# Kernel tuning notes

Measured on AMD Instinct MI355X. Metric: run time of the kernel, lower is better.

## Reference

```python
import jax, jax.numpy as jnp
import numpy as np

B, N, T, F_IN, H, OUT = 64, 207, 48, 6, 64, 1
RANK = 24  # fixed inner dim of learned adjacency factors


def setup_inputs() -> dict:
    key = jax.random.key(0)
    ks = jax.random.split(key, 10)
    s = lambda k, shp, sc=1.0: jax.random.normal(k, shp, jnp.float32) * sc
    return {
        "x": s(ks[0], (B, N, T, F_IN)),
        "N1": s(ks[1], (N, RANK)),
        "N2": s(ks[2], (RANK, N)),
        "W1": s(ks[3], (F_IN, H), 0.2),
        "b1": jnp.zeros((H,), jnp.float32),
        "W2": s(ks[4], (H, H), 0.1),
        "b2": jnp.zeros((H,), jnp.float32),
        "W_ih": s(ks[5], (4 * H, H), 0.1),
        "W_hh": s(ks[6], (4 * H, H), 0.1),
        "b_ih": jnp.zeros((4 * H,), jnp.float32),
        "b_hh": jnp.zeros((4 * H,), jnp.float32),
        "W_fc": s(ks[7], (H, OUT), 0.1),
        "b_fc": jnp.zeros((OUT,), jnp.float32),
    }


def reference(x, N1, N2, W1, b1, W2, b2, W_ih, W_hh, b_ih, b_hh, W_fc, b_fc):
    Bn, Nn, Tn, Fn = x.shape
    # sigmoid(N1@N2) > 0 everywhere -> dense_to_sparse yields ALL N^2 edges
    # (self-loops included); GCNConv's gcn_norm adds one extra self-loop,
    # edge weights all 1 -> A = ones + I, deg = N+1, symmetric normalization.
    adj = jax.nn.sigmoid(N1 @ N2)
    mask = (adj > 0).astype(x.dtype)  # structurally all-ones
    A = mask + jnp.eye(Nn, dtype=x.dtype)
    dinv = jax.lax.rsqrt(A.sum(axis=1))
    A_hat = dinv[:, None] * A * dinv[None, :]  # [N, N]

    xt = jnp.transpose(x, (0, 2, 1, 3))  # [B, T, N, F]
    # GCNConv: propagate(x @ W) with sym-norm, then bias; relu; dropout=eval no-op
    h = jax.nn.relu(jnp.einsum('mn,btnh->btmh', A_hat, xt @ W1) + b1)
    h = jax.nn.relu(jnp.einsum('mn,btnh->btmh', A_hat, h @ W2) + b2)

    # [B, T, N, H] -> [B*N, T, H] for the LSTM
    seq = jnp.transpose(h, (0, 2, 1, 3)).reshape(Bn * Nn, Tn, -1)
    Hd = W_hh.shape[1]

    def step(carry, x_t):
        h_prev, c_prev = carry
        g = x_t @ W_ih.T + b_ih + h_prev @ W_hh.T + b_hh
        i, f, gg, o = jnp.split(g, 4, axis=-1)  # torch gate order i,f,g,o
        c = jax.nn.sigmoid(f) * c_prev + jax.nn.sigmoid(i) * jnp.tanh(gg)
        h_new = jax.nn.sigmoid(o) * jnp.tanh(c)
        return (h_new, c), None

    h0 = jnp.zeros((Bn * Nn, Hd), x.dtype)
    (hT, _), _ = jax.lax.scan(step, (h0, h0), jnp.transpose(seq, (1, 0, 2)))
    out = hT @ W_fc + b_fc  # [B*N, OUT]
    return out.reshape(Bn, Nn, -1)
```

## Files before the change

kernel.cpp:

```cpp
#include <hip/hip_runtime.h>
#include <math.h>

#define NB 64
#define NN 207
#define NT 48
#define NF 6
#define NH 64
#define NSEQ (NB*NN)
#define NG   (NSEQ/16)
#define TSU  ((size_t)NSEQ*NH)

typedef short bf8_t __attribute__((ext_vector_type(8)));
typedef float f4_t  __attribute__((ext_vector_type(4)));
typedef unsigned short ushort;
typedef unsigned int uint;

__device__ __forceinline__ ushort bf16h(float x){
  uint u = __float_as_uint(x);
  return (ushort)((u + 0x7FFF + ((u>>16)&1)) >> 16);
}
__device__ __forceinline__ float bf16f(ushort h){
  return __uint_as_float((uint)h << 16);
}
__device__ __forceinline__ float fsig(float x){
  return __builtin_amdgcn_rcpf(1.0f + __expf(-x));
}
__device__ __forceinline__ float ftanh(float x){
  x = fminf(15.0f, fmaxf(-15.0f, x));
  float e = __expf(2.0f*x);
  return 1.0f - 2.0f*__builtin_amdgcn_rcpf(e + 1.0f);
}

__device__ __forceinline__ void lds_barrier(){
  __builtin_amdgcn_sched_barrier(0);
  asm volatile("s_waitcnt lgkmcnt(0)" ::: "memory");
  __builtin_amdgcn_s_barrier();
  __builtin_amdgcn_sched_barrier(0);
}


#define HW 72
#define XS6 40
#define GCN7_LDS_BYTES (208*HW*2 + (207*XS6 + NF*64 + 64 + 64 + 6*64 + 6*64 + 48)*4)

__global__ __launch_bounds__(256, 2) void gcn_kernel(
    const float* __restrict__ x, const float* __restrict__ W1, const float* __restrict__ b1,
    const float* __restrict__ W2, const float* __restrict__ b2,
    ushort* __restrict__ sxh, ushort* __restrict__ sxl)
{
  extern __shared__ char smraw[];
  ushort* h1b = (ushort*)smraw;
  float*  xs6 = (float*)(h1b + 208*HW);
  float*  W1s = xs6 + 207*XS6;
  float*  b1s = W1s + NF*64;
  float*  b2s = b1s + 64;
  float*  S2_ = b2s + 64;
  float*  r1_ = S2_ + 6*64;
  float*  xsA = r1_ + 6*64;

  const int tid = threadIdx.x;
  const int tg = blockIdx.x, b = blockIdx.y;
  const float inv = 1.0f/208.0f;
  const int l = tid & 63;
  const int w = __builtin_amdgcn_readfirstlane(tid >> 6);
  const int col = l & 15, q = l >> 4;
  const int cw = w*16 + col;

  for (int i=tid; i<6*64; i+=256){ S2_[i]=0.f; r1_[i]=0.f; }
  if (tid < 48) xsA[tid] = 0.f;
  if (tid < 72) h1b[207*HW + tid] = 0;

  for (int i=tid;i<NF*64;i+=256) W1s[i]=W1[i];
  if (tid<64){ b1s[tid]=b1[tid]; b2s[tid]=b2[tid]; }
  {
    const float* xb = x + (size_t)b*NN*(NT*NF) + (size_t)tg*36;
    for (int i=tid; i<207*9; i+=256){
      int n = i/9, c = (i - n*9)*4;
      *(float4*)&xs6[n*XS6 + c] = *(const float4*)&xb[(size_t)n*(NT*NF) + c];
    }
  }
  __syncthreads();

  if (tid < 144){
    int tt = tid/24, rem = tid - tt*24, f = rem>>2, p = rem&3;
    float ps = 0.f;
    for (int n=p; n<NN; n+=4) ps += xs6[n*XS6 + tt*6 + f];
    atomicAdd(&xsA[tt*8+f], ps);
  }

  float wtmp[16];
  #pragma unroll
  for (int kc=0;kc<2;kc++)
    #pragma unroll
    for (int j=0;j<8;j++)
      wtmp[kc*8+j] = W2[(size_t)(kc*32 + q*8 + j)*64 + cw];
  bf8_t B2[2];
  #pragma unroll
  for (int kc=0;kc<2;kc++){
    bf8_t ph;
    #pragma unroll
    for (int j=0;j<8;j++) ph[j] = (short)bf16h(wtmp[kc*8+j]);
    B2[kc]=ph;
  }
  __syncthreads();

  const int ht4 = (tid & 15) * 4;
  const int nti = tid >> 4;

  #pragma unroll 1
  for (int tt=0; tt<6; tt++){
    const int t = tg*6 + tt;
    {
      float s1v[4];
      #pragma unroll
      for (int j=0;j<4;j++){
        float a = 0.f;
        #pragma unroll
        for (int f=0;f<NF;f++) a += xsA[tt*8+f]*W1s[f*64 + ht4 + j];
        s1v[j] = a;
      }
      float cs0=0.f, cs1=0.f, cs2=0.f, cs3=0.f;
      #pragma unroll 1
      for (int p=0;p<4;p++){
        int nt = p*16 + nti;
        if (nt < 52){
          #pragma unroll
          for (int i=0;i<4;i++){
            int n = 4*nt+i;
            if (n < NN){
              float a0=0.f,a1=0.f,a2=0.f,a3=0.f;
              #pragma unroll
              for (int f=0;f<NF;f++){
                float xv = xs6[n*XS6 + tt*6 + f];
                float4 wv = *(const float4*)&W1s[f*64 + ht4];
                a0+=xv*wv.x; a1+=xv*wv.y; a2+=xv*wv.z; a3+=xv*wv.w;
              }
              float v0=(a0+s1v[0])*inv + b1s[ht4+0]; v0 = v0>0.f?v0:0.f;
              float v1=(a1+s1v[1])*inv + b1s[ht4+1]; v1 = v1>0.f?v1:0.f;
              float v2=(a2+s1v[2])*inv + b1s[ht4+2]; v2 = v2>0.f?v2:0.f;
              float v3=(a3+s1v[3])*inv + b1s[ht4+3]; v3 = v3>0.f?v3:0.f;
              ushort4 hi;
              hi.x=bf16h(v0); hi.y=bf16h(v1); hi.z=bf16h(v2); hi.w=bf16h(v3);
              *(ushort4*)&h1b[n*HW + ht4] = hi;
              cs0+=v0; cs1+=v1; cs2+=v2; cs3+=v3;
            }
          }
        }
      }
      atomicAdd(&r1_[tt*64+ht4+0], cs0);
      atomicAdd(&r1_[tt*64+ht4+1], cs1);
      atomicAdd(&r1_[tt*64+ht4+2], cs2);
      atomicAdd(&r1_[tt*64+ht4+3], cs3);
    }
    __syncthreads();

    {
      int h = tid & 63, pp = tid >> 6;
      float ps = 0.f;
      #pragma unroll
      for (int k=0;k<16;k++) ps += r1_[tt*64+pp*16+k]*W2[(size_t)(pp*16+k)*64 + h];
      atomicAdd(&S2_[tt*64+h], ps);
    }

    f4_t acc[13];
    #pragma unroll
    for (int mt=0;mt<13;mt++){ f4_t z; z[0]=0.f;z[1]=0.f;z[2]=0.f;z[3]=0.f; acc[mt]=z; }
    #pragma unroll 2
    for (int mt=0;mt<13;mt++){
      #pragma unroll
      for (int kc=0;kc<2;kc++){
        bf8_t ah = *(const bf8_t*)(h1b + (mt*16+col)*HW + kc*32 + q*8);
        acc[mt] = __builtin_amdgcn_mfma_f32_16x16x32_bf16(ah, B2[kc], acc[mt], 0,0,0);
      }
    }
    __syncthreads();

    {
      const float s2v = S2_[tt*64+cw], b2v = b2s[cw];
      const size_t obase = (size_t)t*TSU + (size_t)(b*NN)*NH + cw;
      #pragma unroll
      for (int mt=0;mt<13;mt++){
        #pragma unroll
        for (int r=0;r<4;r++){
          int n = mt*16 + q*4 + r;
          if (n < NN){
            float v = (acc[mt][r] + s2v)*inv + b2v;
            v = v>0.f ? v : 0.f;
            ushort hb = bf16h(v);
            sxh[obase + (size_t)n*NH] = hb;
            sxl[obase + (size_t)n*NH] = bf16h(v - bf16f(hb));
          }
        }
      }
    }
  }
}

#define HS2 72

__global__ __launch_bounds__(256, 2) void lstm17_kernel(
    const ushort* __restrict__ sxh, const ushort* __restrict__ sxl,
    const float* __restrict__ Wih, const float* __restrict__ Whh,
    const float* __restrict__ bih, const float* __restrict__ bhh,
    const float* __restrict__ Wfc, const float* __restrict__ bfc, float* __restrict__ out)
{
  __shared__ __align__(16) ushort hhp[2][16*HS2 + 8];
  __shared__ __align__(16) ushort hlp[2][16*HS2 + 8];

  const int tid = threadIdx.x;
  const int l = tid & 63;
  const int w = __builtin_amdgcn_readfirstlane(tid >> 6);
  const int col = l & 15, q = l >> 4;
  const int g = blockIdx.x;

  bf8_t Bh[4][4], Bl[4][4];
  #pragma unroll
  for (int mat=0; mat<2; mat++){
    const float* W = mat ? Whh : Wih;
    #pragma unroll
    for (int ty=0; ty<4; ty++){
      #pragma unroll
      for (int kk=0; kk<2; kk++){
        const float* wp = W + (size_t)(ty*64 + w*16 + col)*64 + kk*32 + q*8;
        bf8_t ph, pl;
        #pragma unroll
        for (int j=0;j<8;j++){
          float wv = wp[j];
          ushort hb = bf16h(wv);
          ph[j] = (short)hb;
          pl[j] = (short)bf16h(wv - bf16f(hb));
        }
        Bh[ty][mat*2+kk] = ph;
        Bl[ty][mat*2+kk] = pl;
      }
    }
  }
  float bias[4];
  #pragma unroll
  for (int ty=0;ty<4;ty++){
    int r = ty*64 + w*16 + col;
    bias[ty] = bih[r] + bhh[r];
  }
  float c[4];
  #pragma unroll
  for (int i=0;i<4;i++) c[i]=0.f;

  for (int i=tid; i<16*HS2; i+=256){ hhp[0][i] = 0; hlp[0][i] = 0; }

  const ushort* xgh = sxh + (size_t)g*1024 + (size_t)(col*64 + q*8);
  const ushort* xgl = sxl + (size_t)g*1024 + (size_t)(col*64 + q*8);

  bf8_t pxh[2][2], pxl[2][2];
  #pragma unroll
  for (int s2=0; s2<2; s2++){
    const size_t off = (size_t)s2*TSU;
    pxh[s2][0] = *(const bf8_t*)(xgh + off);
    pxh[s2][1] = *(const bf8_t*)(xgh + off + 32);
    pxl[s2][0] = *(const bf8_t*)(xgl + off);
    pxl[s2][1] = *(const bf8_t*)(xgl + off + 32);
  }

  const int d = w*16 + col;
  __syncthreads();

  #pragma unroll 2
  for (int t=0; t<NT; t++){
    const int cur = t & 1;
    bf8_t cxh0 = pxh[cur][0], cxh1 = pxh[cur][1];
    bf8_t cxl0 = pxl[cur][0], cxl1 = pxl[cur][1];
    if (t+2 < NT){
      const size_t off = (size_t)(t+2)*TSU;
      pxh[cur][0] = *(const bf8_t*)(xgh + off);
      pxh[cur][1] = *(const bf8_t*)(xgh + off + 32);
      pxl[cur][0] = *(const bf8_t*)(xgl + off);
      pxl[cur][1] = *(const bf8_t*)(xgl + off + 32);
    }

    f4_t acc[4];
    #pragma unroll
    for (int ty=0;ty<4;ty++){ f4_t z; z[0]=bias[ty];z[1]=bias[ty];z[2]=bias[ty];z[3]=bias[ty]; acc[ty]=z; }
    #pragma unroll
    for (int ty=0;ty<4;ty++){
      acc[ty] = __builtin_amdgcn_mfma_f32_16x16x32_bf16(cxh0, Bh[ty][0], acc[ty], 0,0,0);
      acc[ty] = __builtin_amdgcn_mfma_f32_16x16x32_bf16(cxl0, Bh[ty][0], acc[ty], 0,0,0);
      acc[ty] = __builtin_amdgcn_mfma_f32_16x16x32_bf16(cxh0, Bl[ty][0], acc[ty], 0,0,0);
      acc[ty] = __builtin_amdgcn_mfma_f32_16x16x32_bf16(cxh1, Bh[ty][1], acc[ty], 0,0,0);
      acc[ty] = __builtin_amdgcn_mfma_f32_16x16x32_bf16(cxl1, Bh[ty][1], acc[ty], 0,0,0);
      acc[ty] = __builtin_amdgcn_mfma_f32_16x16x32_bf16(cxh1, Bl[ty][1], acc[ty], 0,0,0);
    }

    lds_barrier();

    bf8_t hh0, hh1, hl0, hl1;
    {
      const ushort* ph = &hhp[cur][0] + col*HS2 + q*8;
      const ushort* pl = &hlp[cur][0] + col*HS2 + q*8;
      hh0 = *(const bf8_t*)(ph);
      hh1 = *(const bf8_t*)(ph + 32);
      hl0 = *(const bf8_t*)(pl);
      hl1 = *(const bf8_t*)(pl + 32);
    }
    #pragma unroll
    for (int ty=0;ty<4;ty++){
      acc[ty] = __builtin_amdgcn_mfma_f32_16x16x32_bf16(hh0, Bh[ty][2], acc[ty], 0,0,0);
      acc[ty] = __builtin_amdgcn_mfma_f32_16x16x32_bf16(hl0, Bh[ty][2], acc[ty], 0,0,0);
      acc[ty] = __builtin_amdgcn_mfma_f32_16x16x32_bf16(hh0, Bl[ty][2], acc[ty], 0,0,0);
      acc[ty] = __builtin_amdgcn_mfma_f32_16x16x32_bf16(hh1, Bh[ty][3], acc[ty], 0,0,0);
      acc[ty] = __builtin_amdgcn_mfma_f32_16x16x32_bf16(hl1, Bh[ty][3], acc[ty], 0,0,0);
      acc[ty] = __builtin_amdgcn_mfma_f32_16x16x32_bf16(hh1, Bl[ty][3], acc[ty], 0,0,0);
    }

    {
      ushort* wh = &hhp[cur^1][0];
      ushort* wl = &hlp[cur^1][0];
      float hv[4];
      #pragma unroll
      for (int r=0;r<4;r++){
        float ig = fsig(acc[0][r]);
        float fg = fsig(acc[1][r]);
        float gt = ftanh(acc[2][r]);
        float og = fsig(acc[3][r]);
        float cc = fg*c[r] + ig*gt;
        c[r] = cc;
        hv[r] = og*ftanh(cc);
      }
      const int o0 = (q*4)*HS2 + d;
      if (t != NT-1){
        uint ph01, ph23, pl01, pl23;
        asm("v_cvt_pk_bf16_f32 %0, %1, %2" : "=v"(ph01) : "v"(hv[0]), "v"(hv[1]));
        asm("v_cvt_pk_bf16_f32 %0, %1, %2" : "=v"(ph23) : "v"(hv[2]), "v"(hv[3]));
        float r0 = hv[0] - __uint_as_float(ph01 << 16);
        float r1 = hv[1] - __uint_as_float(ph01 & 0xffff0000u);
        float r2 = hv[2] - __uint_as_float(ph23 << 16);
        float r3 = hv[3] - __uint_as_float(ph23 & 0xffff0000u);
        asm("v_cvt_pk_bf16_f32 %0, %1, %2" : "=v"(pl01) : "v"(r0), "v"(r1));
        asm("v_cvt_pk_bf16_f32 %0, %1, %2" : "=v"(pl23) : "v"(r2), "v"(r3));
        wh[o0]         = (ushort)ph01;
        wh[o0 + HS2]   = (ushort)(ph01 >> 16);
        wh[o0 + 2*HS2] = (ushort)ph23;
        wh[o0 + 3*HS2] = (ushort)(ph23 >> 16);
        wl[o0]         = (ushort)pl01;
        wl[o0 + HS2]   = (ushort)(pl01 >> 16);
        wl[o0 + 2*HS2] = (ushort)pl23;
        wl[o0 + 3*HS2] = (ushort)(pl23 >> 16);
      } else {
        #pragma unroll
        for (int r=0;r<4;r++){
          uint bits = __float_as_uint(hv[r]);
          wh[o0 + r*HS2] = (ushort)(bits >> 16);
          wl[o0 + r*HS2] = (ushort)(bits & 0xffffu);
        }
      }
    }
  }
  __syncthreads();

  if (tid < 16){
    float a = bfc[0];
    const ushort* fh = &hhp[NT&1][0] + tid*HS2;
    const ushort* fl = &hlp[NT&1][0] + tid*HS2;
    #pragma unroll 8
    for (int k=0;k<64;k++){
      float v = __uint_as_float(((uint)fh[k] << 16) | (uint)fl[k]);
      a += v * Wfc[k];
    }
    out[g*16 + tid] = a;
  }
}

extern "C" void kernel_launch(void* const* d_in, const int* in_sizes, int n_in,
                              void* d_out, int out_size, void* d_ws, size_t ws_size,
                              hipStream_t stream) {
  const float* x   = (const float*)d_in[0];
  const float* W1  = (const float*)d_in[3];
  const float* b1  = (const float*)d_in[4];
  const float* W2  = (const float*)d_in[5];
  const float* b2  = (const float*)d_in[6];
  const float* Wih = (const float*)d_in[7];
  const float* Whh = (const float*)d_in[8];
  const float* bih = (const float*)d_in[9];
  const float* bhh = (const float*)d_in[10];
  const float* Wfc = (const float*)d_in[11];
  const float* bfc = (const float*)d_in[12];

  ushort* sxh = (ushort*)d_ws;
  ushort* sxl = sxh + (size_t)NT*TSU;
  float*  out = (float*)d_out;

  hipFuncSetAttribute((const void*)gcn_kernel, hipFuncAttributeMaxDynamicSharedMemorySize, GCN7_LDS_BYTES);

  gcn_kernel<<<dim3(NT/6, NB), 256, GCN7_LDS_BYTES, stream>>>(x, W1, b1, W2, b2, sxh, sxl);
  lstm17_kernel<<<NG, 256, 0, stream>>>(sxh, sxl, Wih, Whh, bih, bhh, Wfc, bfc, out);
}
```

Measured before the change: 321.0 us.

## Process two 16-sequence groups per LSTM block with LDS-staged inputs

```diff
diff --git a/kernel.cpp b/kernel.cpp
--- a/kernel.cpp
+++ b/kernel.cpp
@@ -7,7 +7,7 @@
 #define NF 6
 #define NH 64
 #define NSEQ (NB*NN)
-#define NG   (NSEQ/16)
+#define NG2  (NSEQ/32)
 #define TSU  ((size_t)NSEQ*NH)
 
 typedef short bf8_t __attribute__((ext_vector_type(8)));
@@ -198,14 +198,15 @@
 
 #define HS2 72
 
-__global__ __launch_bounds__(256, 2) void lstm17_kernel(
+__global__ __launch_bounds__(256, 2) void lstm19_kernel(
     const ushort* __restrict__ sxh, const ushort* __restrict__ sxl,
     const float* __restrict__ Wih, const float* __restrict__ Whh,
     const float* __restrict__ bih, const float* __restrict__ bhh,
     const float* __restrict__ Wfc, const float* __restrict__ bfc, float* __restrict__ out)
 {
-  __shared__ __align__(16) ushort hhp[2][16*HS2 + 8];
-  __shared__ __align__(16) ushort hlp[2][16*HS2 + 8];
+  __shared__ __align__(16) ushort hhp[2][2][16*HS2 + 8];
+  __shared__ __align__(16) ushort hlp[2][2][16*HS2 + 8];
+  __shared__ __align__(16) ushort xst[2][2][2][2][512];
 
   const int tid = threadIdx.x;
   const int l = tid & 63;
@@ -222,16 +223,16 @@
       #pragma unroll
       for (int kk=0; kk<2; kk++){
         const float* wp = W + (size_t)(ty*64 + w*16 + col)*64 + kk*32 + q*8;
-        bf8_t ph, pl;
+        bf8_t ph, pl2;
         #pragma unroll
         for (int j=0;j<8;j++){
           float wv = wp[j];
           ushort hb = bf16h(wv);
           ph[j] = (short)hb;
-          pl[j] = (short)bf16h(wv - bf16f(hb));
+          pl2[j] = (short)bf16h(wv - bf16f(hb));
         }
         Bh[ty][mat*2+kk] = ph;
-        Bl[ty][mat*2+kk] = pl;
+        Bl[ty][mat*2+kk] = pl2;
       }
     }
   }
@@ -241,23 +242,25 @@
     int r = ty*64 + w*16 + col;
     bias[ty] = bih[r] + bhh[r];
   }
-  float c[4];
-  #pragma unroll
-  for (int i=0;i<4;i++) c[i]=0.f;
-
-  for (int i=tid; i<16*HS2; i+=256){ hhp[0][i] = 0; hlp[0][i] = 0; }
-
-  const ushort* xgh = sxh + (size_t)g*1024 + (size_t)(col*64 + q*8);
-  const ushort* xgl = sxl + (size_t)g*1024 + (size_t)(col*64 + q*8);
-
-  bf8_t pxh[2][2], pxl[2][2];
-  #pragma unroll
-  for (int s2=0; s2<2; s2++){
-    const size_t off = (size_t)s2*TSU;
-    pxh[s2][0] = *(const bf8_t*)(xgh + off);
-    pxh[s2][1] = *(const bf8_t*)(xgh + off + 32);
-    pxl[s2][0] = *(const bf8_t*)(xgl + off);
-    pxl[s2][1] = *(const bf8_t*)(xgl + off + 32);
+  float c[2][4];
+  #pragma unroll
+  for (int s=0;s<2;s++)
+    #pragma unroll
+    for (int i=0;i<4;i++) c[s][i]=0.f;
+
+  for (int i=tid; i<16*HS2; i+=256){
+    hhp[0][0][i]=0; hhp[0][1][i]=0; hlp[0][0][i]=0; hlp[0][1][i]=0;
+  }
+
+  const int ss = w >> 1, pl = w & 1;
+  const ushort* xsrc = (pl ? sxl : sxh) + (size_t)(g*32 + ss*16 + col)*64 + (size_t)(q*8);
+
+  #pragma unroll
+  for (int t2=0; t2<2; t2++){
+    bf8_t a0 = *(const bf8_t*)(xsrc + (size_t)t2*TSU);
+    bf8_t a1 = *(const bf8_t*)(xsrc + (size_t)t2*TSU + 32);
+    *(bf8_t*)&xst[t2][ss][pl][0][l*8] = a0;
+    *(bf8_t*)&xst[t2][ss][pl][1][l*8] = a1;
   }
 
   const int d = w*16 + col;
@@ -266,62 +269,82 @@
   #pragma unroll 2
   for (int t=0; t<NT; t++){
     const int cur = t & 1;
-    bf8_t cxh0 = pxh[cur][0], cxh1 = pxh[cur][1];
-    bf8_t cxl0 = pxl[cur][0], cxl1 = pxl[cur][1];
-    if (t+2 < NT){
-      const size_t off = (size_t)(t+2)*TSU;
-      pxh[cur][0] = *(const bf8_t*)(xgh + off);
-      pxh[cur][1] = *(const bf8_t*)(xgh + off + 32);
-      pxl[cur][0] = *(const bf8_t*)(xgl + off);
-      pxl[cur][1] = *(const bf8_t*)(xgl + off + 32);
-    }
-
-    f4_t acc[4];
-    #pragma unroll
-    for (int ty=0;ty<4;ty++){ f4_t z; z[0]=bias[ty];z[1]=bias[ty];z[2]=bias[ty];z[3]=bias[ty]; acc[ty]=z; }
-    #pragma unroll
-    for (int ty=0;ty<4;ty++){
-      acc[ty] = __builtin_amdgcn_mfma_f32_16x16x32_bf16(cxh0, Bh[ty][0], acc[ty], 0,0,0);
-      acc[ty] = __builtin_amdgcn_mfma_f32_16x16x32_bf16(cxl0, Bh[ty][0], acc[ty], 0,0,0);
-      acc[ty] = __builtin_amdgcn_mfma_f32_16x16x32_bf16(cxh0, Bl[ty][0], acc[ty], 0,0,0);
-      acc[ty] = __builtin_amdgcn_mfma_f32_16x16x32_bf16(cxh1, Bh[ty][1], acc[ty], 0,0,0);
-      acc[ty] = __builtin_amdgcn_mfma_f32_16x16x32_bf16(cxl1, Bh[ty][1], acc[ty], 0,0,0);
-      acc[ty] = __builtin_amdgcn_mfma_f32_16x16x32_bf16(cxh1, Bl[ty][1], acc[ty], 0,0,0);
-    }
+
+    bf8_t g0, g1;
+    const bool do_stage = (t+2 < NT);
+    if (do_stage){
+      g0 = *(const bf8_t*)(xsrc + (size_t)(t+2)*TSU);
+      g1 = *(const bf8_t*)(xsrc + (size_t)(t+2)*TSU + 32);
+    }
+
+    bf8_t xh0[2], xh1[2], xl0[2], xl1[2];
+    #pragma unroll
+    for (int s=0;s<2;s++){
+      xh0[s] = *(const bf8_t*)&xst[cur][s][0][0][l*8];
+      xh1[s] = *(const bf8_t*)&xst[cur][s][0][1][l*8];
+      xl0[s] = *(const bf8_t*)&xst[cur][s][1][0][l*8];
+      xl1[s] = *(const bf8_t*)&xst[cur][s][1][1][l*8];
+    }
+
+    f4_t acc[2][4];
+    #pragma unroll
+    for (int s=0;s<2;s++)
+      #pragma unroll
+      for (int ty=0;ty<4;ty++){ f4_t z; z[0]=bias[ty];z[1]=bias[ty];z[2]=bias[ty];z[3]=bias[ty]; acc[s][ty]=z; }
+    #pragma unroll
+    for (int s=0;s<2;s++)
+      #pragma unroll
+      for (int ty=0;ty<4;ty++){
+        acc[s][ty] = __builtin_amdgcn_mfma_f32_16x16x32_bf16(xh0[s], Bh[ty][0], acc[s][ty], 0,0,0);
+        acc[s][ty] = __builtin_amdgcn_mfma_f32_16x16x32_bf16(xl0[s], Bh[ty][0], acc[s][ty], 0,0,0);
+        acc[s][ty] = __builtin_amdgcn_mfma_f32_16x16x32_bf16(xh0[s], Bl[ty][0], acc[s][ty], 0,0,0);
+        acc[s][ty] = __builtin_amdgcn_mfma_f32_16x16x32_bf16(xh1[s], Bh[ty][1], acc[s][ty], 0,0,0);
+        acc[s][ty] = __builtin_amdgcn_mfma_f32_16x16x32_bf16(xl1[s], Bh[ty][1], acc[s][ty], 0,0,0);
+        acc[s][ty] = __builtin_amdgcn_mfma_f32_16x16x32_bf16(xh1[s], Bl[ty][1], acc[s][ty], 0,0,0);
+      }
 
     lds_barrier();
 
-    bf8_t hh0, hh1, hl0, hl1;
-    {
-      const ushort* ph = &hhp[cur][0] + col*HS2 + q*8;
-      const ushort* pl = &hlp[cur][0] + col*HS2 + q*8;
-      hh0 = *(const bf8_t*)(ph);
-      hh1 = *(const bf8_t*)(ph + 32);
-      hl0 = *(const bf8_t*)(pl);
-      hl1 = *(const bf8_t*)(pl + 32);
-    }
-    #pragma unroll
-    for (int ty=0;ty<4;ty++){
-      acc[ty] = __builtin_amdgcn_mfma_f32_16x16x32_bf16(hh0, Bh[ty][2], acc[ty], 0,0,0);
-      acc[ty] = __builtin_amdgcn_mfma_f32_16x16x32_bf16(hl0, Bh[ty][2], acc[ty], 0,0,0);
-      acc[ty] = __builtin_amdgcn_mfma_f32_16x16x32_bf16(hh0, Bl[ty][2], acc[ty], 0,0,0);
-      acc[ty] = __builtin_amdgcn_mfma_f32_16x16x32_bf16(hh1, Bh[ty][3], acc[ty], 0,0,0);
-      acc[ty] = __builtin_amdgcn_mfma_f32_16x16x32_bf16(hl1, Bh[ty][3], acc[ty], 0,0,0);
-      acc[ty] = __builtin_amdgcn_mfma_f32_16x16x32_bf16(hh1, Bl[ty][3], acc[ty], 0,0,0);
-    }
-
-    {
-      ushort* wh = &hhp[cur^1][0];
-      ushort* wl = &hlp[cur^1][0];
+    bf8_t hh0[2], hh1[2], hl0[2], hl1[2];
+    #pragma unroll
+    for (int s=0;s<2;s++){
+      const ushort* ph = &hhp[cur][s][0] + col*HS2 + q*8;
+      const ushort* pl2 = &hlp[cur][s][0] + col*HS2 + q*8;
+      hh0[s] = *(const bf8_t*)(ph);
+      hh1[s] = *(const bf8_t*)(ph + 32);
+      hl0[s] = *(const bf8_t*)(pl2);
+      hl1[s] = *(const bf8_t*)(pl2 + 32);
+    }
+    #pragma unroll
+    for (int s=0;s<2;s++)
+      #pragma unroll
+      for (int ty=0;ty<4;ty++){
+        acc[s][ty] = __builtin_amdgcn_mfma_f32_16x16x32_bf16(hh0[s], Bh[ty][2], acc[s][ty], 0,0,0);
+        acc[s][ty] = __builtin_amdgcn_mfma_f32_16x16x32_bf16(hl0[s], Bh[ty][2], acc[s][ty], 0,0,0);
+        acc[s][ty] = __builtin_amdgcn_mfma_f32_16x16x32_bf16(hh0[s], Bl[ty][2], acc[s][ty], 0,0,0);
+        acc[s][ty] = __builtin_amdgcn_mfma_f32_16x16x32_bf16(hh1[s], Bh[ty][3], acc[s][ty], 0,0,0);
+        acc[s][ty] = __builtin_amdgcn_mfma_f32_16x16x32_bf16(hl1[s], Bh[ty][3], acc[s][ty], 0,0,0);
+        acc[s][ty] = __builtin_amdgcn_mfma_f32_16x16x32_bf16(hh1[s], Bl[ty][3], acc[s][ty], 0,0,0);
+      }
+
+    if (do_stage){
+      *(bf8_t*)&xst[cur][ss][pl][0][l*8] = g0;
+      *(bf8_t*)&xst[cur][ss][pl][1][l*8] = g1;
+    }
+
+    #pragma unroll
+    for (int s=0;s<2;s++){
+      ushort* wh = &hhp[cur^1][s][0];
+      ushort* wl = &hlp[cur^1][s][0];
       float hv[4];
       #pragma unroll
       for (int r=0;r<4;r++){
-        float ig = fsig(acc[0][r]);
-        float fg = fsig(acc[1][r]);
-        float gt = ftanh(acc[2][r]);
-        float og = fsig(acc[3][r]);
-        float cc = fg*c[r] + ig*gt;
-        c[r] = cc;
+        float ig = fsig(acc[s][0][r]);
+        float fg = fsig(acc[s][1][r]);
+        float gt = ftanh(acc[s][2][r]);
+        float og = fsig(acc[s][3][r]);
+        float cc = fg*c[s][r] + ig*gt;
+        c[s][r] = cc;
         hv[r] = og*ftanh(cc);
       }
       const int o0 = (q*4)*HS2 + d;
@@ -355,16 +378,17 @@
   }
   __syncthreads();
 
-  if (tid < 16){
+  if (tid < 32){
+    const int s = tid >> 4, r = tid & 15;
     float a = bfc[0];
-    const ushort* fh = &hhp[NT&1][0] + tid*HS2;
-    const ushort* fl = &hlp[NT&1][0] + tid*HS2;
+    const ushort* fh = &hhp[NT&1][s][0] + r*HS2;
+    const ushort* fl = &hlp[NT&1][s][0] + r*HS2;
     #pragma unroll 8
     for (int k=0;k<64;k++){
       float v = __uint_as_float(((uint)fh[k] << 16) | (uint)fl[k]);
       a += v * Wfc[k];
     }
-    out[g*16 + tid] = a;
+    out[g*32 + tid] = a;
   }
 }
 
@@ -390,5 +414,5 @@
   hipFuncSetAttribute((const void*)gcn_kernel, hipFuncAttributeMaxDynamicSharedMemorySize, GCN7_LDS_BYTES);
 
   gcn_kernel<<<dim3(NT/6, NB), 256, GCN7_LDS_BYTES, stream>>>(x, W1, b1, W2, b2, sxh, sxl);
-  lstm17_kernel<<<NG, 256, 0, stream>>>(sxh, sxl, Wih, Whh, bih, bhh, Wfc, bfc, out);
-}
+  lstm19_kernel<<<NG2, 256, 0, stream>>>(sxh, sxl, Wih, Whh, bih, bhh, Wfc, bfc, out);
+}
```

Measured after the change: 304.5 us. 1.05x faster.
